# Kernel optimization log

Hardware: AMD Instinct MI355X
Metric: run time of the kernel (lower is better)

Reference implementation:

```python
import jax, jax.numpy as jnp
import numpy as np

B, FIN, V, X, Y, Z = 2, 32, 768, 8, 8, 8
K, FOUT = 5, 32
NNZ = V * 8  # ~8 neighbors per vertex


def setup_inputs() -> dict:
    key = jax.random.key(0)
    k1, k2, k3, k4, k5 = jax.random.split(key, 5)
    std = np.sqrt(2.0 / (FIN * K)).astype(np.float32)
    return {
        "lap_rows": jax.random.randint(k1, (NNZ,), 0, V, dtype=jnp.int32),
        "lap_cols": jax.random.randint(k2, (NNZ,), 0, V, dtype=jnp.int32),
        "lap_vals": jax.random.normal(k3, (NNZ,), dtype=jnp.float32) * 0.1,
        "x": jax.random.normal(k4, (B, FIN, V, X, Y, Z), dtype=jnp.float32),
        "weight": jax.random.normal(k5, (K, FIN, FOUT), dtype=jnp.float32) * std,
        "bias": jnp.full((FOUT,), 0.01, dtype=jnp.float32),
    }


def reference(lap_rows, lap_cols, lap_vals, x, weight, bias):
    Bb, Fin, Vv, Xx, Yy, Zz = x.shape
    Kk, _, Fout = weight.shape

    def spmm(v):  # sparse [V,V] @ dense [V,D]
        return jax.ops.segment_sum(lap_vals[:, None] * v[lap_cols],
                                   lap_rows, num_segments=Vv)

    # [B,Fin,V,X,Y,Z] -> [V, Fin*B*X*Y*Z]
    x0 = jnp.transpose(x, (2, 1, 0, 3, 4, 5)).reshape(Vv, -1)
    xs = [x0]
    if Kk > 1:
        x1 = spmm(x0)
        xs.append(x1)
        for _ in range(2, Kk):
            x2 = 2.0 * spmm(x1) - x0
            xs.append(x2)
            x0, x1 = x1, x2
    basis = jnp.stack(xs, axis=0)  # [K, V, Fin*B*X*Y*Z]
    basis = basis.reshape(Kk, Vv, Fin, Bb, Xx, Yy, Zz)
    basis = jnp.transpose(basis, (3, 1, 4, 5, 6, 0, 2))  # [B,V,X,Y,Z,K,Fin]
    out = basis.reshape(-1, Kk * Fin) @ weight.reshape(Kk * Fin, Fout)
    out = out.reshape(Bb, Vv, Xx, Yy, Zz, Fout)
    out = jnp.transpose(out, (0, 5, 1, 2, 3, 4))  # [B,Fout,V,X,Y,Z]
    return out + bias[None, :, None, None, None, None]
```

## Files before the change

### kernel.cpp

```cpp
#include <hip/hip_runtime.h>
#include <stdint.h>

#define V      768
#define FINC   32
#define FOUTC  32
#define XYZ    512
#define NB     2
#define ROWP   40
#define MAXDEG 32
#define EROWS  (MAXDEG + 2)

typedef unsigned short u16;
typedef unsigned int   u32;
typedef short bf16x8 __attribute__((ext_vector_type(8)));
typedef float f32x4  __attribute__((ext_vector_type(4)));
typedef float f32x2  __attribute__((ext_vector_type(2)));

__device__ __forceinline__ u16 f2bf(float f) {
  u32 u = __float_as_uint(f);
  u32 r = u + 0x7fffu + ((u >> 16) & 1u);
  return (u16)(r >> 16);
}
__device__ __forceinline__ float bflo(u32 w) { return __uint_as_float(w << 16); }
__device__ __forceinline__ float bfhi(u32 w) { return __uint_as_float(w & 0xffff0000u); }
__device__ __forceinline__ float bfhi_raw(u32 w) { return __uint_as_float(w); }
__device__ __forceinline__ u32 cvtpk_bf16(float lo, float hi) {
  u32 r;
  asm("v_cvt_pk_bf16_f32 %0, %1, %2" : "=v"(r) : "v"(lo), "v"(hi));
  return r;
}

__global__ __launch_bounds__(64) void build_ell(const int* __restrict__ rows,
                                                const int* __restrict__ cols,
                                                const float* __restrict__ vals,
                                                int nnz,
                                                int2* __restrict__ epair,
                                                int* __restrict__ deg) {
  int v = blockIdx.x;
  int lane = threadIdx.x;
  int cnt = 0;
  for (int base = 0; base < nnz; base += 64) {
    int i = base + lane;
    bool m = (i < nnz) && (rows[i] == v);
    unsigned long long mask = __ballot(m);
    if (m) {
      int pos = cnt + __popcll(mask & ((1ull << lane) - 1ull));
      if (pos < MAXDEG)
        epair[v * MAXDEG + pos] = make_int2(cols[i], __float_as_int(vals[i]));
    }
    cnt += __popcll(mask);
  }
  int d = cnt < MAXDEG ? cnt : MAXDEG;
  for (int p = d + lane; p < MAXDEG; p += 64)
    epair[v * MAXDEG + p] = make_int2(0, 0);
  if (lane == 0) deg[v] = d;
}

__global__ __launch_bounds__(V) void sort_rows(const int2* __restrict__ epair,
                                               const int* __restrict__ deg,
                                               int2* __restrict__ ep3,
                                               int* __restrict__ perm,
                                               int* __restrict__ inv_g,
                                               int* __restrict__ wtrip) {
  __shared__ int sdeg[V];
  __shared__ u16 sinv[V];
  int v = threadIdx.x;
  int d = deg[v];
  sdeg[v] = d;
  __syncthreads();
  int r = 0;
  for (int u = 0; u < V; ++u) {
    int du = sdeg[u];
    r += (du > d) || (du == d && u < v);
  }
  const unsigned long long GPK = 0x8495A6B73210ull;
  int w = (int)((GPK >> (4 * (r >> 6))) & 15ull);
  int p = w * 64 + (r & 63);
  perm[p] = v;
  inv_g[v] = p;
  sinv[v] = (u16)p;
  if ((r & 63) == 0) wtrip[w] = d;
  __syncthreads();
  for (int e = 0; e < EROWS; ++e) {
    int2 o = make_int2(0, 0);
    if (e < d) {
      int2 pe = epair[v * MAXDEG + e];
      o = make_int2((int)sinv[pe.x] * (ROWP * 2), pe.y);
    }
    ep3[e * V + p] = o;
  }
}

#define TXV 12
__global__ __launch_bounds__(512) void transpose_x(const float* __restrict__ x,
                                                   const int* __restrict__ perm,
                                                   u16* __restrict__ xT) {
  __shared__ u16 TL[384][66];
  __shared__ int PV[TXV];
  int g = blockIdx.x;
  int b = g >> 9, pvt = (g >> 3) & 63, xt = g & 7;
  int pv0 = pvt * TXV;
  int xyz0 = xt * 64;
  int t = threadIdx.x;
  if (t < TXV) PV[t] = perm[pv0 + t];
  __syncthreads();
  int lane = t & 63, pg = t >> 6;
#pragma unroll
  for (int st = 0; st < 48; ++st) {
    int pair = st * 8 + pg;
    int vloc = pair >> 5, f = pair & 31;
    float val = x[((size_t)(b * FINC + f) * V + PV[vloc]) * XYZ + xyz0 + lane];
    TL[pair][lane] = f2bf(val);
  }
  __syncthreads();
  int s = t & 7, xyz = t >> 3;
  u32* dst = (u32*)(xT + ((size_t)(b * XYZ + xyz0 + xyz) * V + pv0) * FINC);
#pragma unroll
  for (int it = 0; it < 24; ++it) {
    int i = s + 8 * it;
    u32 lo = TL[2 * i][xyz], hi = TL[2 * i + 1][xyz];
    dst[i] = lo | (hi << 16);
  }
}

__global__ __launch_bounds__(1024, 4) void cheb_main(
    const u16* __restrict__ xT, const int2* __restrict__ ep3,
    const int* __restrict__ perm, const int* __restrict__ wtrip,
    const float* __restrict__ weight, const float* __restrict__ bias,
    u32* __restrict__ stage) {
  __shared__ __align__(16) u16   CUR[V * ROWP];
  __shared__ __align__(16) uint4 WF[5][2][64];
  __shared__ u16 PRM[V];
  __shared__ int WT[12];

  int g = blockIdx.x;
  int xcd = g & 7;
  int u = g >> 3;
  int phase = u >> 5;
  int xyz = xcd * 32 + (u & 31) + (phase & 1) * 256;
  int b = phase >> 1;
  int slice = b * XYZ + xyz;

  int tid = threadIdx.x;
  int lane = tid & 63;
  int w = tid >> 6;
  int l15 = lane & 15, l4 = lane >> 4;
  bool gath = tid < V;

  if (tid < 640) {
    int k = tid >> 7, n = (tid >> 6) & 1, ln = tid & 63;
    int a15 = ln & 15, a4 = ln >> 4;
    u32 pw[4];
#pragma unroll
    for (int p = 0; p < 4; ++p) {
      float w0 = weight[(size_t)(k * FINC + a4 * 8 + 2 * p) * FOUTC + n * 16 + a15];
      float w1 = weight[(size_t)(k * FINC + a4 * 8 + 2 * p + 1) * FOUTC + n * 16 + a15];
      pw[p] = (u32)f2bf(w0) | ((u32)f2bf(w1) << 16);
    }
    WF[k][n][ln] = make_uint4(pw[0], pw[1], pw[2], pw[3]);
  }
  if (tid < 12) WT[tid] = wtrip[tid];
  if (gath) PRM[tid] = (u16)perm[tid];
  float bsv[2] = {bias[l15], bias[16 + l15]};

  u32 curpk[16], prevpk[16];
  if (gath) {
    const uint4* src = (const uint4*)(xT + (size_t)slice * V * FINC) + tid * 4;
    uint4* dst = (uint4*)(CUR + tid * ROWP);
#pragma unroll
    for (int j = 0; j < 4; ++j) {
      uint4 q = src[j];
      dst[j] = q;
      curpk[4 * j] = q.x; curpk[4 * j + 1] = q.y;
      curpk[4 * j + 2] = q.z; curpk[4 * j + 3] = q.w;
    }
  }
  __syncthreads();

  int trip = 0;
  if (w < 12) trip = __builtin_amdgcn_readfirstlane(WT[w]);
  const int2* pp = ep3 + tid;

  f32x4 acc[3][2];
#pragma unroll
  for (int a = 0; a < 3; ++a)
#pragma unroll
    for (int n = 0; n < 2; ++n) acc[a][n] = (f32x4){0.f, 0.f, 0.f, 0.f};

  auto gemm_acc = [&](int k) {
    bf16x8 bn0 = *(const bf16x8*)&WF[k][0][lane];
    bf16x8 bn1 = *(const bf16x8*)&WF[k][1][lane];
#pragma unroll
    for (int a = 0; a < 3; ++a) {
      int row = w * 48 + a * 16 + l15;
      bf16x8 af = *(const bf16x8*)(CUR + row * ROWP + l4 * 8);
      acc[a][0] = __builtin_amdgcn_mfma_f32_16x16x32_bf16(af, bn0, acc[a][0], 0, 0, 0);
      acc[a][1] = __builtin_amdgcn_mfma_f32_16x16x32_bf16(af, bn1, acc[a][1], 0, 0, 0);
    }
  };

  f32x2 fa2[16];
  auto gather = [&]() {
#pragma unroll
    for (int j = 0; j < 16; ++j) fa2[j] = (f32x2){0.f, 0.f};
    int2 pe0 = pp[0];
    int2 pe1 = pp[V];
    for (int e = 0; e < trip; ++e) {
      int2 nx = pp[(e + 2) * V];
      float fv = __int_as_float(pe0.y);
      f32x2 fv2 = {fv, fv};
      const uint4* sp = (const uint4*)((const char*)CUR + (u32)pe0.x);
      uint4 qa = sp[0], qb = sp[1], qc = sp[2], qd = sp[3];
      u32 wq[16] = {qa.x, qa.y, qa.z, qa.w, qb.x, qb.y, qb.z, qb.w,
                    qc.x, qc.y, qc.z, qc.w, qd.x, qd.y, qd.z, qd.w};
#pragma unroll
      for (int p = 0; p < 16; ++p) {
        f32x2 s = {bflo(wq[p]), bfhi_raw(wq[p])};
        fa2[p] += fv2 * s;
      }
      pe0 = pe1; pe1 = nx;
    }
  };

  auto store_cur = [&]() {
    uint4* dp = (uint4*)(CUR + tid * ROWP);
#pragma unroll
    for (int j = 0; j < 4; ++j)
      dp[j] = make_uint4(curpk[4 * j], curpk[4 * j + 1], curpk[4 * j + 2], curpk[4 * j + 3]);
  };

  gemm_acc(0);
  if (gath) gather();
  __syncthreads();
  if (gath) {
#pragma unroll
    for (int j = 0; j < 16; ++j) {
      prevpk[j] = curpk[j];
      curpk[j] = cvtpk_bf16(fa2[j][0], fa2[j][1]);
    }
    store_cur();
  }
  __syncthreads();

#pragma unroll
  for (int ph = 1; ph <= 3; ++ph) {
    gemm_acc(ph);
    if (gath) gather();
    __syncthreads();
    if (gath) {
#pragma unroll
      for (int j = 0; j < 16; ++j) {
        u32 pv = prevpk[j];
        float t0 = 2.f * fa2[j][0] - bflo(pv);
        float t1 = 2.f * fa2[j][1] - bfhi(pv);
        prevpk[j] = curpk[j];
        curpk[j] = cvtpk_bf16(t0, t1);
      }
      store_cur();
    }
    __syncthreads();
  }

  gemm_acc(4);

  u32* stg = stage + (size_t)slice * (V * 16);
#pragma unroll
  for (int a = 0; a < 3; ++a) {
#pragma unroll
    for (int r = 0; r < 4; ++r) {
      int vr = PRM[w * 48 + a * 16 + l4 * 4 + r];
      u32 pk = cvtpk_bf16(acc[a][0][r] + bsv[0], acc[a][1][r] + bsv[1]);
      stg[vr * 16 + l15] = pk;
    }
  }
}

#define TO_VT  12
#define TO_PAD 193
__global__ __launch_bounds__(512) void transpose_out(const u32* __restrict__ stage,
                                                     float* __restrict__ out) {
  __shared__ u32 T[64 * TO_PAD];
  int g = blockIdx.x;
  int b = g >> 9, vt = (g >> 3) & 63, xt = g & 7;
  int v0 = vt * TO_VT;
  int xyz0 = xt * 64;
  int t = threadIdx.x;
  const u32* base = stage + (size_t)(b * XYZ + xyz0) * (V * 16) + v0 * 16;
#pragma unroll
  for (int i = 0; i < 6; ++i) {
    int idx4 = i * 512 + t;
    int j = idx4 / 48;
    int c4 = idx4 - j * 48;
    uint4 q = *(const uint4*)(base + (size_t)j * (V * 16) + c4 * 4);
    int w0 = c4 * 4;
    T[j * TO_PAD + w0]     = q.x;
    T[j * TO_PAD + w0 + 1] = q.y;
    T[j * TO_PAD + w0 + 2] = q.z;
    T[j * TO_PAD + w0 + 3] = q.w;
  }
  __syncthreads();
  int wv = t >> 6, lane = t & 63;
#pragma unroll
  for (int i = 0; i < 48; ++i) {
    int fout = wv * 4 + i / 12;
    int vv = i % 12;
    u32 pk = T[lane * TO_PAD + vv * 16 + (fout & 15)];
    float val = (fout < 16) ? bflo(pk) : bfhi(pk);
    out[((size_t)(b * FOUTC + fout) * V + v0 + vv) * XYZ + xyz0 + lane] = val;
  }
}

extern "C" void kernel_launch(void* const* d_in, const int* in_sizes, int n_in,
                              void* d_out, int out_size, void* d_ws, size_t ws_size,
                              hipStream_t stream) {
  const int*   lap_rows = (const int*)d_in[0];
  const int*   lap_cols = (const int*)d_in[1];
  const float* lap_vals = (const float*)d_in[2];
  const float* x        = (const float*)d_in[3];
  const float* weight   = (const float*)d_in[4];
  const float* bias     = (const float*)d_in[5];
  float* out = (float*)d_out;
  int nnz = in_sizes[0];

  char* ws = (char*)d_ws;
  const size_t XT_BYTES = (size_t)NB * XYZ * V * FINC * sizeof(u16);
  const size_t EP_BYTES = (size_t)V * MAXDEG * 8;
  const size_t E3_BYTES = (size_t)EROWS * V * 8;
  u16*  xT    = (u16*)ws;
  u32*  stg   = (u32*)ws;
  int2* epair = (int2*)(ws + XT_BYTES);
  int2* ep3   = (int2*)(ws + XT_BYTES + EP_BYTES);
  int*  deg   = (int*)(ws + XT_BYTES + EP_BYTES + E3_BYTES);
  int*  perm  = (int*)(ws + XT_BYTES + EP_BYTES + E3_BYTES + 3072);
  int*  inv_g = (int*)(ws + XT_BYTES + EP_BYTES + E3_BYTES + 6144);
  int*  wtrip = (int*)(ws + XT_BYTES + EP_BYTES + E3_BYTES + 9216);

  hipLaunchKernelGGL(build_ell, dim3(V), dim3(64), 0, stream,
                     lap_rows, lap_cols, lap_vals, nnz, epair, deg);
  hipLaunchKernelGGL(sort_rows, dim3(1), dim3(V), 0, stream,
                     epair, deg, ep3, perm, inv_g, wtrip);
  hipLaunchKernelGGL(transpose_x, dim3(NB * 64 * 8), dim3(512), 0, stream,
                     x, perm, xT);
  hipLaunchKernelGGL(cheb_main, dim3(NB * XYZ), dim3(1024), 0, stream,
                     xT, ep3, perm, wtrip, weight, bias, stg);
  hipLaunchKernelGGL(transpose_out, dim3(NB * 64 * 8), dim3(512), 0, stream,
                     stg, out);
}
```

Baseline: 215.6 us.

## Move Chebyshev prev/cur state to LDS and double-buffer edge gather loads

Per-thread curpk/prevpk register arrays are replaced by a second LDS buffer PRV, and the update reads current and previous rows from LDS before writing them back. The gather loop is unrolled by two, so each iteration has two neighbor rows' LDS loads in flight while the FMAs run; the trip count is rounded up to even and EROWS is raised to 36 to pad the edge table. This is meant to cut register pressure and hide LDS latency. It roughly doubles LDS use per block (an extra 768x40 u16), which could lower occupancy, and it adds LDS traffic in the update step.

```diff
diff --git a/kernel.cpp b/kernel.cpp
--- a/kernel.cpp
+++ b/kernel.cpp
@@ -8,7 +8,7 @@
 #define NB     2
 #define ROWP   40
 #define MAXDEG 32
-#define EROWS  (MAXDEG + 2)
+#define EROWS  36
 
 typedef unsigned short u16;
 typedef unsigned int   u32;
@@ -129,6 +129,7 @@
     const float* __restrict__ weight, const float* __restrict__ bias,
     u32* __restrict__ stage) {
   __shared__ __align__(16) u16   CUR[V * ROWP];
+  __shared__ __align__(16) u16   PRV[V * ROWP];
   __shared__ __align__(16) uint4 WF[5][2][64];
   __shared__ u16 PRM[V];
   __shared__ int WT[12];
@@ -163,17 +164,11 @@
   if (gath) PRM[tid] = (u16)perm[tid];
   float bsv[2] = {bias[l15], bias[16 + l15]};
 
-  u32 curpk[16], prevpk[16];
   if (gath) {
     const uint4* src = (const uint4*)(xT + (size_t)slice * V * FINC) + tid * 4;
     uint4* dst = (uint4*)(CUR + tid * ROWP);
 #pragma unroll
-    for (int j = 0; j < 4; ++j) {
-      uint4 q = src[j];
-      dst[j] = q;
-      curpk[4 * j] = q.x; curpk[4 * j + 1] = q.y;
-      curpk[4 * j + 2] = q.z; curpk[4 * j + 3] = q.w;
-    }
+    for (int j = 0; j < 4; ++j) dst[j] = src[j];
   }
   __syncthreads();
 
@@ -200,64 +195,72 @@
   };
 
   f32x2 fa2[16];
+  auto fma_edge = [&](float fv, uint4 qa, uint4 qb, uint4 qc, uint4 qd) {
+    f32x2 fv2 = {fv, fv};
+    u32 wq[16] = {qa.x, qa.y, qa.z, qa.w, qb.x, qb.y, qb.z, qb.w,
+                  qc.x, qc.y, qc.z, qc.w, qd.x, qd.y, qd.z, qd.w};
+#pragma unroll
+    for (int p = 0; p < 16; ++p) {
+      f32x2 s = {bflo(wq[p]), bfhi_raw(wq[p])};
+      fa2[p] += fv2 * s;
+    }
+  };
   auto gather = [&]() {
 #pragma unroll
     for (int j = 0; j < 16; ++j) fa2[j] = (f32x2){0.f, 0.f};
-    int2 pe0 = pp[0];
-    int2 pe1 = pp[V];
-    for (int e = 0; e < trip; ++e) {
-      int2 nx = pp[(e + 2) * V];
-      float fv = __int_as_float(pe0.y);
-      f32x2 fv2 = {fv, fv};
-      const uint4* sp = (const uint4*)((const char*)CUR + (u32)pe0.x);
-      uint4 qa = sp[0], qb = sp[1], qc = sp[2], qd = sp[3];
-      u32 wq[16] = {qa.x, qa.y, qa.z, qa.w, qb.x, qb.y, qb.z, qb.w,
-                    qc.x, qc.y, qc.z, qc.w, qd.x, qd.y, qd.z, qd.w};
-#pragma unroll
-      for (int p = 0; p < 16; ++p) {
-        f32x2 s = {bflo(wq[p]), bfhi_raw(wq[p])};
-        fa2[p] += fv2 * s;
+    int trips = (trip + 1) & ~1;
+    int2 r0 = pp[0], r1 = pp[V], r2 = pp[2 * V];
+    const uint4* s0 = (const uint4*)((const char*)CUR + (u32)r0.x);
+    uint4 A0 = s0[0], A1 = s0[1], A2 = s0[2], A3 = s0[3];
+    for (int e = 0; e < trips; e += 2) {
+      const uint4* s1 = (const uint4*)((const char*)CUR + (u32)r1.x);
+      uint4 B0 = s1[0], B1 = s1[1], B2 = s1[2], B3 = s1[3];
+      int2 n3 = pp[(e + 3) * V];
+      fma_edge(__int_as_float(r0.y), A0, A1, A2, A3);
+      const uint4* s2 = (const uint4*)((const char*)CUR + (u32)r2.x);
+      A0 = s2[0]; A1 = s2[1]; A2 = s2[2]; A3 = s2[3];
+      int2 n4 = pp[(e + 4) * V];
+      fma_edge(__int_as_float(r1.y), B0, B1, B2, B3);
+      r0 = r2; r1 = n3; r2 = n4;
+    }
+  };
+
+  auto do_update = [&](bool first) {
+    uint4* cp = (uint4*)(CUR + tid * ROWP);
+    uint4* qp = (uint4*)(PRV + tid * ROWP);
+    uint4 c[4];
+#pragma unroll
+    for (int j = 0; j < 4; ++j) c[j] = cp[j];
+    u32 npk[16];
+    if (first) {
+#pragma unroll
+      for (int j = 0; j < 16; ++j) npk[j] = cvtpk_bf16(fa2[j][0], fa2[j][1]);
+    } else {
+      uint4 pv[4];
+#pragma unroll
+      for (int j = 0; j < 4; ++j) pv[j] = qp[j];
+      u32 wp[16] = {pv[0].x, pv[0].y, pv[0].z, pv[0].w, pv[1].x, pv[1].y, pv[1].z, pv[1].w,
+                    pv[2].x, pv[2].y, pv[2].z, pv[2].w, pv[3].x, pv[3].y, pv[3].z, pv[3].w};
+#pragma unroll
+      for (int j = 0; j < 16; ++j) {
+        float t0 = 2.f * fa2[j][0] - bflo(wp[j]);
+        float t1 = 2.f * fa2[j][1] - bfhi(wp[j]);
+        npk[j] = cvtpk_bf16(t0, t1);
       }
-      pe0 = pe1; pe1 = nx;
+    }
+#pragma unroll
+    for (int j = 0; j < 4; ++j) {
+      qp[j] = c[j];
+      cp[j] = make_uint4(npk[4 * j], npk[4 * j + 1], npk[4 * j + 2], npk[4 * j + 3]);
     }
   };
 
-  auto store_cur = [&]() {
-    uint4* dp = (uint4*)(CUR + tid * ROWP);
-#pragma unroll
-    for (int j = 0; j < 4; ++j)
-      dp[j] = make_uint4(curpk[4 * j], curpk[4 * j + 1], curpk[4 * j + 2], curpk[4 * j + 3]);
-  };
-
-  gemm_acc(0);
-  if (gath) gather();
-  __syncthreads();
-  if (gath) {
-#pragma unroll
-    for (int j = 0; j < 16; ++j) {
-      prevpk[j] = curpk[j];
-      curpk[j] = cvtpk_bf16(fa2[j][0], fa2[j][1]);
-    }
-    store_cur();
-  }
-  __syncthreads();
-
-#pragma unroll
-  for (int ph = 1; ph <= 3; ++ph) {
+#pragma unroll
+  for (int ph = 0; ph <= 3; ++ph) {
     gemm_acc(ph);
     if (gath) gather();
     __syncthreads();
-    if (gath) {
-#pragma unroll
-      for (int j = 0; j < 16; ++j) {
-        u32 pv = prevpk[j];
-        float t0 = 2.f * fa2[j][0] - bflo(pv);
-        float t1 = 2.f * fa2[j][1] - bfhi(pv);
-        prevpk[j] = curpk[j];
-        curpk[j] = cvtpk_bf16(t0, t1);
-      }
-      store_cur();
-    }
+    if (gath) do_update(ph == 0);
     __syncthreads();
   }
 
```

Measured after the change: 204.6 us. 5.1% less time.
